# Optimization experiments

Measured on AMD Instinct MI355X. Metric: run time of the kernel, lower is better.

Reference implementation:

```python
import jax, jax.numpy as jnp
import numpy as np
import math

BS, S, D = 2, 2048, 2048
DOWN, UP, H, RD = 512, 1024, 16, 32
HD = D // H            # 128, used only in softmax scale
VD = UP // H           # 64 per-head value dim
CD = UP // H           # 64 per-head content q/k dim
SCALE = math.sqrt(HD) + math.sqrt(RD)


def _rope(x, head_dim):
    # x: [bs, heads, seq, head_dim]; standard rotate-half RoPE
    seq = x.shape[2]
    inv_freq = 1.0 / (10000.0 ** (jnp.arange(0, head_dim, 2, dtype=jnp.float32) / head_dim))
    freqs = jnp.arange(seq, dtype=jnp.float32)[:, None] * inv_freq[None, :]  # [S, hd/2]
    emb = jnp.concatenate([freqs, freqs], axis=-1)                            # [S, hd]
    cos = jnp.cos(emb)[None, None]
    sin = jnp.sin(emb)[None, None]
    x1, x2 = x[..., : head_dim // 2], x[..., head_dim // 2 :]
    rot = jnp.concatenate([-x2, x1], axis=-1)
    return x * cos + rot * sin


def setup_inputs() -> dict:
    key = jax.random.key(0)
    ks = jax.random.split(key, 10)
    sd = 0.02
    inp = {
        'h': jax.random.normal(ks[0], (BS, S, D), jnp.float32),
        'mask': jnp.tril(jnp.ones((1, 1, S, S), jnp.int32)),
        'Wdkv': jax.random.normal(ks[1], (DOWN, D), jnp.float32) * sd,
        'bdkv': jnp.zeros((DOWN,), jnp.float32),
        'Wuk': jax.random.normal(ks[2], (UP, DOWN), jnp.float32) * sd,
        'buk': jnp.zeros((UP,), jnp.float32),
        'Wuv': jax.random.normal(ks[3], (UP, DOWN), jnp.float32) * sd,
        'buv': jnp.zeros((UP,), jnp.float32),
        'Wdq': jax.random.normal(ks[4], (DOWN, D), jnp.float32) * sd,
        'bdq': jnp.zeros((DOWN,), jnp.float32),
        'Wuq': jax.random.normal(ks[5], (UP, DOWN), jnp.float32) * sd,
        'buq': jnp.zeros((UP,), jnp.float32),
        'Wqr': jax.random.normal(ks[6], (RD * H, DOWN), jnp.float32) * sd,
        'bqr': jnp.zeros((RD * H,), jnp.float32),
        'Wkr': jax.random.normal(ks[7], (RD, D), jnp.float32) * sd,
        'bkr': jnp.zeros((RD,), jnp.float32),
        'Wfc': jax.random.normal(ks[8], (D, H * VD), jnp.float32) * sd,
        'bfc': jnp.zeros((D,), jnp.float32),
    }
    return inp


def reference(h, mask, Wdkv, bdkv, Wuk, buk, Wuv, buv, Wdq, bdq, Wuq, buq,
              Wqr, bqr, Wkr, bkr, Wfc, bfc):
    bs, seq, _ = h.shape
    # low-rank KV path
    c_kv = h @ Wdkv.T + bdkv                                   # [bs,S,DOWN]
    k_c = (c_kv @ Wuk.T + buk).reshape(bs, seq, H, CD).transpose(0, 2, 1, 3)
    v_c = (c_kv @ Wuv.T + buv).reshape(bs, seq, H, VD).transpose(0, 2, 1, 3)
    # low-rank Q path
    c_q = h @ Wdq.T + bdq                                      # [bs,S,DOWN]
    q_c = (c_q @ Wuq.T + buq).reshape(bs, seq, H, CD).transpose(0, 2, 1, 3)
    # decoupled RoPE paths
    q_r = _rope((c_q @ Wqr.T + bqr).reshape(bs, seq, H, RD).transpose(0, 2, 1, 3), RD)
    k_r = _rope((h @ Wkr.T + bkr).reshape(bs, seq, 1, RD).transpose(0, 2, 1, 3), RD)
    k_r = jnp.broadcast_to(k_r, (bs, H, seq, RD))              # shared RoPE key across heads
    q = jnp.concatenate([q_c, q_r], axis=-1)                   # [bs,H,S,CD+RD]
    k = jnp.concatenate([k_c, k_r], axis=-1)
    scores = jnp.einsum('bhqd,bhkd->bhqk', q, k)
    # NB: original applies mask BEFORE dividing by scale
    scores = jnp.where(mask == 0, -1e9, scores)
    probs = jax.nn.softmax(scores / SCALE, axis=-1)
    out = jnp.einsum('bhqk,bhkd->bhqd', probs, v_c)            # [bs,H,S,VD]
    out = out.transpose(0, 2, 1, 3).reshape(bs, seq, H * VD)
    return out @ Wfc.T + bfc
```

## Files before the change

### kernel.cpp

```cpp
#include <hip/hip_runtime.h>
#include <hip/hip_bf16.h>
#include <math.h>

typedef unsigned short u16;
typedef __attribute__((ext_vector_type(8))) short bf16x8;
typedef __attribute__((ext_vector_type(4))) float f32x4;
typedef __attribute__((ext_vector_type(16))) float f32x16;

namespace {

constexpr int BS = 2;
constexpr int S = 2048;
constexpr int D = 2048;
constexpr int DOWN = 512;
constexpr int UP = 1024;
constexpr int H = 16;
constexpr int RD = 32;
constexpr int VD = 64;
constexpr int QKD = 96;
constexpr int M = BS * S;
constexpr int N1 = 1152;
constexpr int N2 = 2048;
constexpr int N3 = 1536;

__device__ __forceinline__ float b2f(u16 u) {
  unsigned int x = ((unsigned int)u) << 16;
  return __uint_as_float(x);
}
__device__ __forceinline__ u16 f2b(float f) {
  unsigned int u = __float_as_uint(f);
  u += 0x7fff + ((u >> 16) & 1);
  return (u16)(u >> 16);
}
__device__ __forceinline__ void store_out(float* p, float v) { *p = v; }
__device__ __forceinline__ void store_out(u16* p, float v) { *p = f2b(v); }

__device__ __forceinline__ void async16(const u16* g, u16* lds) {
  __builtin_amdgcn_global_load_lds(
      (const __attribute__((address_space(1))) unsigned int*)g,
      (__attribute__((address_space(3))) unsigned int*)lds, 16, 0, 0);
}

__device__ __forceinline__ float exp2_fast(float x) {
#if __has_builtin(__builtin_amdgcn_exp2f)
  return __builtin_amdgcn_exp2f(x);
#else
  float r;
  asm("v_exp_f32 %0, %1" : "=v"(r) : "v"(x));
  return r;
#endif
}

__device__ __forceinline__ unsigned pkbf(float a, float b) {
  union { __hip_bfloat162 h; unsigned u; } c;
  c.h = __float22bfloat162_rn(make_float2(a, b));
  return c.u;
}
__device__ __forceinline__ void plswap(unsigned& a, unsigned& b) {
  asm("v_permlane32_swap_b32 %0, %1" : "+v"(a), "+v"(b));
}

__device__ __forceinline__ f32x4 mfma32(bf16x8 a, bf16x8 b, f32x4 c) {
  return __builtin_amdgcn_mfma_f32_16x16x32_bf16(a, b, c, 0, 0, 0);
}
__device__ __forceinline__ f32x16 mfma3216(bf16x8 a, bf16x8 b, f32x16 c) {
  return __builtin_amdgcn_mfma_f32_32x32x16_bf16(a, b, c, 0, 0, 0);
}

__global__ __launch_bounds__(256) void prep_kernel(
    const float* __restrict__ h, const float* __restrict__ Wdkv,
    const float* __restrict__ Wdq, const float* __restrict__ Wkr,
    const float* __restrict__ Wuk, const float* __restrict__ Wuv,
    const float* __restrict__ Wuq, const float* __restrict__ Wqr,
    const float* __restrict__ Wfc, const float* __restrict__ bdkv,
    const float* __restrict__ bdq, const float* __restrict__ bkr,
    const float* __restrict__ buk, const float* __restrict__ buv,
    const float* __restrict__ buq, const float* __restrict__ bqr,
    u16* __restrict__ hb, u16* __restrict__ Wcat1, u16* __restrict__ Wcat2,
    u16* __restrict__ Wcat3, u16* __restrict__ Wfcb,
    float* __restrict__ bcat1, float* __restrict__ bcat2,
    float* __restrict__ bcat3, float* __restrict__ ct, float* __restrict__ st) {
  const long i = (long)blockIdx.x * 256 + threadIdx.x;
  if (i >= 3630240) return;
  if (i < 3620864) {
    const float* src; u16* dst; long off;
    if      (i < 2097152) { src = h;    dst = hb;              off = i; }
    else if (i < 2359296) { src = Wdkv; dst = Wcat1;           off = i - 2097152; }
    else if (i < 2621440) { src = Wdq;  dst = Wcat1 + 1048576; off = i - 2359296; }
    else if (i < 2637824) { src = Wkr;  dst = Wcat1 + 2097152; off = i - 2621440; }
    else if (i < 2768896) { src = Wuk;  dst = Wcat2;           off = i - 2637824; }
    else if (i < 2899968) { src = Wuv;  dst = Wcat2 + 524288;  off = i - 2768896; }
    else if (i < 3031040) { src = Wuq;  dst = Wcat3;           off = i - 2899968; }
    else if (i < 3096576) { src = Wqr;  dst = Wcat3 + 524288;  off = i - 3031040; }
    else                  { src = Wfc;  dst = Wfcb;            off = i - 3096576; }
    float4 v = ((const float4*)src)[off];
    ushort4 o;
    o.x = f2b(v.x); o.y = f2b(v.y); o.z = f2b(v.z); o.w = f2b(v.w);
    ((ushort4*)dst)[off] = o;
  } else if (i < 3622048) {
    long j0 = (i - 3620864) * 4;
#pragma unroll
    for (int e = 0; e < 4; ++e) {
      long j = j0 + e;
      if (j < N1) {
        float v = 0.f;
        if (j < 512) v = bdkv[j];
        else if (j < 1024) v = bdq[j - 512];
        else if (j < 1056) v = bkr[j - 1024];
        bcat1[j] = v;
      } else if (j < N1 + N2) {
        long jj = j - N1;
        bcat2[jj] = (jj < 1024) ? buk[jj] : buv[jj - 1024];
      } else {
        long jj = j - N1 - N2;
        bcat3[jj] = (jj < 1024) ? buq[jj] : bqr[jj - 1024];
      }
    }
  } else {
    long k0 = (i - 3622048) * 4;
#pragma unroll
    for (int e = 0; e < 4; ++e) {
      long k = k0 + e;
      int s = (int)(k >> 4), r = (int)(k & 15);
      float f = powf(10000.f, -(float)r / 16.f);
      float th = (float)s * f;
      ct[k] = cosf(th);
      st[k] = sinf(th);
    }
  }
}

template <int BN, typename OutT>
__device__ __forceinline__ void gemm_body(
    const u16* __restrict__ A, int lda, const u16* __restrict__ W, int ldw,
    const float* __restrict__ bias, OutT* __restrict__ C, int ldc, int K,
    int m0, int n0) {
  constexpr int NFR = BN / 32;
  __shared__ u16 As[128 * 32];
  __shared__ u16 Bs[BN * 32];
  const int t = threadIdx.x;
  const int lane = t & 63, wave = t >> 6;
  const int wm = (wave >> 1) * 64, wn = (wave & 1) * (BN / 2);
  const int lrow = lane & 15, lk = (lane >> 4) * 8;
  const int srow = lane >> 2, scol = (lane & 3) * 8;
  f32x4 acc[4][NFR] = {};
  for (int k0 = 0; k0 < K; k0 += 32) {
    __syncthreads();
    {
      int r = wave * 32 + srow;
      async16(A + (size_t)(m0 + r) * lda + k0 + scol, As + (wave * 32) * 32);
      async16(A + (size_t)(m0 + r + 16) * lda + k0 + scol,
              As + (wave * 32 + 16) * 32);
    }
    if (BN == 128) {
      int r = wave * 32 + srow;
      async16(W + (size_t)(n0 + r) * ldw + k0 + scol, Bs + (wave * 32) * 32);
      async16(W + (size_t)(n0 + r + 16) * ldw + k0 + scol,
              Bs + (wave * 32 + 16) * 32);
    } else {
      int r = wave * 16 + srow;
      async16(W + (size_t)(n0 + r) * ldw + k0 + scol, Bs + (wave * 16) * 32);
    }
    __syncthreads();
    bf16x8 af[4], bfr[NFR];
#pragma unroll
    for (int i = 0; i < 4; ++i)
      af[i] = *(const bf16x8*)(As + (wm + i * 16 + lrow) * 32 + lk);
#pragma unroll
    for (int i = 0; i < NFR; ++i)
      bfr[i] = *(const bf16x8*)(Bs + (wn + i * 16 + lrow) * 32 + lk);
#pragma unroll
    for (int mi = 0; mi < 4; ++mi)
#pragma unroll
      for (int ni = 0; ni < NFR; ++ni)
        acc[mi][ni] = mfma32(af[mi], bfr[ni], acc[mi][ni]);
  }
#pragma unroll
  for (int mi = 0; mi < 4; ++mi)
#pragma unroll
    for (int ni = 0; ni < NFR; ++ni)
#pragma unroll
      for (int r = 0; r < 4; ++r) {
        int m = m0 + wm + mi * 16 + (lane >> 4) * 4 + r;
        int n = n0 + wn + ni * 16 + lrow;
        store_out(C + (size_t)m * ldc + n, acc[mi][ni][r] + bias[n]);
      }
}

template <int BN, typename OutT>
__global__ __launch_bounds__(256) void gemm_bt_mfma(
    const u16* __restrict__ A, int lda, const u16* __restrict__ W, int ldw,
    const float* __restrict__ bias, OutT* __restrict__ C, int ldc, int K) {
  gemm_body<BN, OutT>(A, lda, W, ldw, bias, C, ldc, K,
                      blockIdx.x * 128, blockIdx.y * BN);
}

__global__ __launch_bounds__(256) void gemm_up_fused(
    const u16* __restrict__ C1v, const u16* __restrict__ Wcat2,
    const u16* __restrict__ Wcat3, const float* __restrict__ bcat2,
    const float* __restrict__ bcat3, u16* __restrict__ C2,
    u16* __restrict__ C3) {
  const int by = blockIdx.y;
  const u16* A;
  const u16* W;
  const float* bias;
  u16* C;
  int ldc, n0;
  if (by < 16) {
    A = C1v; W = Wcat2; bias = bcat2; C = C2; ldc = N2; n0 = by * 128;
  } else {
    A = C1v + DOWN; W = Wcat3; bias = bcat3; C = C3; ldc = N3;
    n0 = (by - 16) * 128;
  }
  gemm_body<128, u16>(A, N1, W, DOWN, bias, C, ldc, DOWN,
                      blockIdx.x * 128, n0);
}

__global__ __launch_bounds__(256) void transpose_v_kernel(
    const u16* __restrict__ in, int ld_in, u16* __restrict__ VtB) {
  __shared__ u16 tile[64][72];
  const int m0 = blockIdx.x * 64;
  const int h = blockIdx.y;
  const int r = threadIdx.x >> 2, c0 = (threadIdx.x & 3) * 16;
  *(bf16x8*)(&tile[r][c0]) =
      *(const bf16x8*)(in + (size_t)(m0 + r) * ld_in + h * VD + c0);
  *(bf16x8*)(&tile[r][c0 + 8]) =
      *(const bf16x8*)(in + (size_t)(m0 + r) * ld_in + h * VD + c0 + 8);
  __syncthreads();
  bf16x8 o0, o1;
#pragma unroll
  for (int j = 0; j < 8; ++j) {
    o0[j] = (short)tile[c0 + j][r];
    o1[j] = (short)tile[c0 + 8 + j][r];
  }
  const int b = m0 / S, sb = m0 % S;
  size_t dst = ((size_t)(b * H + h) * 64 + ((sb + c0) >> 5)) * 2048 +
               (size_t)r * 32 + ((sb + c0) & 31);
  *(bf16x8*)(VtB + dst) = o0;
  *(bf16x8*)(VtB + dst + 8) = o1;
}

__global__ __launch_bounds__(192) void pack_q_kernel(
    const u16* __restrict__ qc, const u16* __restrict__ qr,
    const float* __restrict__ ct, const float* __restrict__ st,
    u16* __restrict__ Qp) {
  const int t = threadIdx.x;
  const int sub = (t >= 96) ? 1 : 0;
  const int d = t - sub * 96;
  const int s = blockIdx.x * 2 + sub, h = blockIdx.y, b = blockIdx.z;
  const float sc = 1.44269504088896f / (sqrtf(128.f) + sqrtf(32.f));
  float val;
  if (d < 64) {
    val = b2f(qc[(size_t)(b * S + s) * N3 + h * VD + d]);
  } else {
    int r = d - 64;
    const u16* qrow = qr + (size_t)(b * S + s) * N3 + h * RD;
    float x = b2f(qrow[r]), xp = b2f(qrow[r ^ 16]);
    float c = ct[s * 16 + (r & 15)], sn = st[s * 16 + (r & 15)];
    val = (r < 16) ? (x * c - xp * sn) : (x * c + xp * sn);
  }
  Qp[((size_t)(b * H + h) * S + s) * QKD + d] = f2b(val * sc);
}

__global__ __launch_bounds__(192) void pack_k_kernel(
    const u16* __restrict__ kc,
    const u16* __restrict__ kr,
    const float* __restrict__ ct, const float* __restrict__ st,
    u16* __restrict__ Kp) {
  const int t = threadIdx.x;
  const int sub = (t >= 96) ? 1 : 0;
  const int d = t - sub * 96;
  const int s = blockIdx.x * 2 + sub, h = blockIdx.y, b = blockIdx.z;
  float val;
  if (d < 64) {
    val = b2f(kc[(size_t)(b * S + s) * N2 + h * VD + d]);
  } else {
    int r = d - 64;
    const u16* krow = kr + (size_t)(b * S + s) * N1;
    float x = b2f(krow[r]), xp = b2f(krow[r ^ 16]);
    float c = ct[s * 16 + (r & 15)], sn = st[s * 16 + (r & 15)];
    val = (r < 16) ? (x * c - xp * sn) : (x * c + xp * sn);
  }
  Kp[((size_t)(b * H + h) * S + s) * QKD + d] = f2b(val);
}

__global__ __launch_bounds__(256, 3) void attn_mfma(
    const u16* __restrict__ Qp, const u16* __restrict__ Kp,
    const u16* __restrict__ Vt, u16* __restrict__ attnb) {
  const int t = threadIdx.x, wave = t >> 6, lane = t & 63;
  const int l31 = lane & 31, hw = lane >> 5;
  const int xcd = (int)(blockIdx.x & 7), sub = (int)(blockIdx.x >> 3);
  const int bh = xcd * 4 + (sub & 3);
  const int tile = 63 - (sub >> 2);
  const int b = bh >> 4, h = bh & 15;
  const int q0w = tile * 32;
  const size_t hbo = (size_t)bh * S;

  __shared__ float red[3][64][33];

  bf16x8 qf[6];
  {
    const u16* qrow = Qp + (hbo + q0w + l31) * QKD + hw * 8;
#pragma unroll
    for (int c = 0; c < 6; ++c) qf[c] = *(const bf16x8*)(qrow + c * 16);
  }
  f32x16 O0 = {0,0,0,0,0,0,0,0,0,0,0,0,0,0,0,0};
  f32x16 O1 = {0,0,0,0,0,0,0,0,0,0,0,0,0,0,0,0};
  float lsum = 0.f;
  const int q_abs = q0w + l31;
  const u16* vbase = Vt + (size_t)bh * 64 * 2048 + l31 * 32 + 8 * hw;
  const u16* kpb = Kp + hbo * QKD;

  auto qk_part1 = [&](bf16x8* kf, f32x16& sa, f32x16& sb) {
    sa = mfma3216(kf[0], qf[0], sa);
    sb = mfma3216(kf[1], qf[1], sb);
    sa = mfma3216(kf[2], qf[2], sa);
    sb = mfma3216(kf[3], qf[3], sb);
    sa = mfma3216(kf[4], qf[4], sa);
    sb = mfma3216(kf[5], qf[5], sb);
  };
  auto finish = [&](const f32x16& sa, const f32x16& sb, const bf16x8* vf,
                    int m) {
    float e[16];
    if (m == tile) {
      const int k0 = m * 32;
#pragma unroll
      for (int r = 0; r < 16; ++r) {
        int key_abs = k0 + (r & 3) + 8 * (r >> 2) + 4 * hw;
        float v = exp2_fast(sa[r] + sb[r]);
        e[r] = (key_abs <= q_abs) ? v : 0.f;
      }
    } else {
#pragma unroll
      for (int r = 0; r < 16; ++r) e[r] = exp2_fast(sa[r] + sb[r]);
    }
    {
      float p0 = (e[0] + e[1]) + (e[2] + e[3]);
      float p1 = (e[4] + e[5]) + (e[6] + e[7]);
      float p2 = (e[8] + e[9]) + (e[10] + e[11]);
      float p3 = (e[12] + e[13]) + (e[14] + e[15]);
      lsum += (p0 + p1) + (p2 + p3);
    }
    unsigned w0 = pkbf(e[0], e[1]),   w1 = pkbf(e[2], e[3]);
    unsigned w2 = pkbf(e[4], e[5]),   w3 = pkbf(e[6], e[7]);
    unsigned w4 = pkbf(e[8], e[9]),   w5 = pkbf(e[10], e[11]);
    unsigned w6 = pkbf(e[12], e[13]), w7 = pkbf(e[14], e[15]);
    plswap(w0, w2); plswap(w1, w3); plswap(w4, w6); plswap(w5, w7);
    union { unsigned u[4]; bf16x8 v; } ua, ub;
    ua.u[0] = w0; ua.u[1] = w1; ua.u[2] = w2; ua.u[3] = w3;
    ub.u[0] = w4; ub.u[1] = w5; ub.u[2] = w6; ub.u[3] = w7;
    O0 = mfma3216(ua.v, vf[0], O0);
    O1 = mfma3216(ua.v, vf[2], O1);
    O0 = mfma3216(ub.v, vf[1], O0);
    O1 = mfma3216(ub.v, vf[3], O1);
  };
  auto loadK = [&](int m, bf16x8* kf) {
    const u16* kb = kpb + (size_t)(m * 32 + l31) * QKD + hw * 8;
#pragma unroll
    for (int c = 0; c < 6; ++c) kf[c] = *(const bf16x8*)(kb + c * 16);
  };
  auto loadV = [&](int m, bf16x8* vf) {
    const u16* vb = vbase + (size_t)m * 2048;
    vf[0] = *(const bf16x8*)(vb);
    vf[1] = *(const bf16x8*)(vb + 16);
    vf[2] = *(const bf16x8*)(vb + 1024);
    vf[3] = *(const bf16x8*)(vb + 1024 + 16);
  };

  if (tile >= wave) {
    bf16x8 kf[6], vfE[4], vfO[4];
    int m = wave;
    loadK(m, kf);
    loadV(m, vfE);
    while (true) {
      {
        if (m + 4 <= tile) loadV(m + 4, vfO);
        f32x16 sa = {0,0,0,0,0,0,0,0,0,0,0,0,0,0,0,0};
        f32x16 sb = {0,0,0,0,0,0,0,0,0,0,0,0,0,0,0,0};
        qk_part1(kf, sa, sb);
        if (m + 4 <= tile) loadK(m + 4, kf);
        finish(sa, sb, vfE, m);
      }
      m += 4;
      if (m > tile) break;
      {
        if (m + 4 <= tile) loadV(m + 4, vfE);
        f32x16 sa = {0,0,0,0,0,0,0,0,0,0,0,0,0,0,0,0};
        f32x16 sb = {0,0,0,0,0,0,0,0,0,0,0,0,0,0,0,0};
        qk_part1(kf, sa, sb);
        if (m + 4 <= tile) loadK(m + 4, kf);
        finish(sa, sb, vfO, m);
      }
      m += 4;
      if (m > tile) break;
    }
  }

  if (wave > 0) {
#pragma unroll
    for (int r = 0; r < 16; ++r) {
      red[wave - 1][lane][r] = O0[r];
      red[wave - 1][lane][16 + r] = O1[r];
    }
    red[wave - 1][lane][32] = lsum;
  }
  __syncthreads();
  if (wave == 0) {
#pragma unroll
    for (int w = 0; w < 3; ++w) {
#pragma unroll
      for (int r = 0; r < 16; ++r) {
        O0[r] += red[w][lane][r];
        O1[r] += red[w][lane][16 + r];
      }
      lsum += red[w][lane][32];
    }
    float tot = lsum + __shfl_xor(lsum, 32);
    u16* ob = attnb + (size_t)b * S * UP + h * VD;
#pragma unroll
    for (int r = 0; r < 16; ++r) {
      int rowq = (r & 3) + 8 * (r >> 2) + 4 * hw;
      float linv = 1.f / __shfl(tot, rowq);
      size_t rowoff = (size_t)(q0w + rowq) * UP;
      ob[rowoff + l31] = f2b(O0[r] * linv);
      ob[rowoff + 32 + l31] = f2b(O1[r] * linv);
    }
  }
}

}

extern "C" void kernel_launch(void* const* d_in, const int* in_sizes, int n_in,
                              void* d_out, int out_size, void* d_ws, size_t ws_size,
                              hipStream_t stream) {
  const float* h    = (const float*)d_in[0];
  const float* Wdkv = (const float*)d_in[2];
  const float* bdkv = (const float*)d_in[3];
  const float* Wuk  = (const float*)d_in[4];
  const float* buk  = (const float*)d_in[5];
  const float* Wuv  = (const float*)d_in[6];
  const float* buv  = (const float*)d_in[7];
  const float* Wdq  = (const float*)d_in[8];
  const float* bdq  = (const float*)d_in[9];
  const float* Wuq  = (const float*)d_in[10];
  const float* buq  = (const float*)d_in[11];
  const float* Wqr  = (const float*)d_in[12];
  const float* bqr  = (const float*)d_in[13];
  const float* Wkr  = (const float*)d_in[14];
  const float* bkr  = (const float*)d_in[15];
  const float* Wfc  = (const float*)d_in[16];
  const float* bfc  = (const float*)d_in[17];
  float* out = (float*)d_out;

  u16* p = (u16*)d_ws;
  u16* hb    = p; p += (size_t)M * D;
  u16* Wcat1 = p; p += (size_t)N1 * D;
  u16* Wcat2 = p; p += (size_t)N2 * DOWN;
  u16* Wcat3 = p; p += (size_t)N3 * DOWN;
  u16* Wfcb  = p; p += (size_t)D * UP;
  u16* C1    = p; p += (size_t)M * N1;
  u16* C2    = p; p += (size_t)M * N2;
  u16* C3    = p; p += (size_t)M * N3;
  u16* Qp    = p; p += 6291456;
  u16* Kp    = p; p += 6291456;
  u16* Vt    = p; p += (size_t)UP * M;
  float* bcat1 = (float*)p; p += 2 * N1;
  float* bcat2 = (float*)p; p += 2 * N2;
  float* bcat3 = (float*)p; p += 2 * N3;
  float* ct = (float*)p; p += 2 * S * 16;
  float* st = (float*)p; p += 2 * S * 16;
  u16* attnb = C1;

  prep_kernel<<<dim3(14181), 256, 0, stream>>>(
      h, Wdkv, Wdq, Wkr, Wuk, Wuv, Wuq, Wqr, Wfc,
      bdkv, bdq, bkr, buk, buv, buq, bqr,
      hb, Wcat1, Wcat2, Wcat3, Wfcb, bcat1, bcat2, bcat3, ct, st);

  gemm_bt_mfma<128, u16><<<dim3(M / 128, N1 / 128), 256, 0, stream>>>(
      hb, D, Wcat1, D, bcat1, C1, N1, D);
  gemm_up_fused<<<dim3(M / 128, 28), 256, 0, stream>>>(
      C1, Wcat2, Wcat3, bcat2, bcat3, C2, C3);

  pack_q_kernel<<<dim3(S / 2, H, BS), 192, 0, stream>>>(
      C3, C3 + UP, ct, st, Qp);
  pack_k_kernel<<<dim3(S / 2, H, BS), 192, 0, stream>>>(
      C2, C1 + 2 * DOWN, ct, st, Kp);
  transpose_v_kernel<<<dim3(M / 64, UP / 64), 256, 0, stream>>>(
      C2 + UP, N2, Vt);

  attn_mfma<<<dim3(2048), 256, 0, stream>>>(Qp, Kp, Vt, attnb);

  gemm_bt_mfma<128, float><<<dim3(M / 128, D / 128), 256, 0, stream>>>(
      attnb, UP, Wfcb, UP, bfc, out, D, UP);
}
```

Baseline: 318.9 us.

## Merge Q/K pack and V transpose kernels, add setprio around MFMAs, shrink GEMM tile

The Q pack, K pack and V transpose kernels become one flat-indexed launch that uses block ranges to pick the work, which removes two launches and their tail effects. The attention kernel wraps its MFMA groups in s_setprio to raise wave priority during matrix work. The first projection GEMM moves to a 64-wide N tile, doubling its grid for better CU occupancy. The flat indexing adds div/mod by 96 per element, and writes are now contiguous per element while reads become scattered.

```diff
diff --git a/kernel.cpp b/kernel.cpp
--- a/kernel.cpp
+++ b/kernel.cpp
@@ -22,6 +22,7 @@
 constexpr int N1 = 1152;
 constexpr int N2 = 2048;
 constexpr int N3 = 1536;
+constexpr long PACK_ELEMS = (long)BS * H * S * QKD;
 
 __device__ __forceinline__ float b2f(u16 u) {
   unsigned int x = ((unsigned int)u) << 16;
@@ -216,72 +217,72 @@
                       blockIdx.x * 128, n0);
 }
 
-__global__ __launch_bounds__(256) void transpose_v_kernel(
-    const u16* __restrict__ in, int ld_in, u16* __restrict__ VtB) {
-  __shared__ u16 tile[64][72];
-  const int m0 = blockIdx.x * 64;
-  const int h = blockIdx.y;
-  const int r = threadIdx.x >> 2, c0 = (threadIdx.x & 3) * 16;
-  *(bf16x8*)(&tile[r][c0]) =
-      *(const bf16x8*)(in + (size_t)(m0 + r) * ld_in + h * VD + c0);
-  *(bf16x8*)(&tile[r][c0 + 8]) =
-      *(const bf16x8*)(in + (size_t)(m0 + r) * ld_in + h * VD + c0 + 8);
-  __syncthreads();
-  bf16x8 o0, o1;
-#pragma unroll
-  for (int j = 0; j < 8; ++j) {
-    o0[j] = (short)tile[c0 + j][r];
-    o1[j] = (short)tile[c0 + 8 + j][r];
-  }
-  const int b = m0 / S, sb = m0 % S;
-  size_t dst = ((size_t)(b * H + h) * 64 + ((sb + c0) >> 5)) * 2048 +
-               (size_t)r * 32 + ((sb + c0) & 31);
-  *(bf16x8*)(VtB + dst) = o0;
-  *(bf16x8*)(VtB + dst + 8) = o1;
-}
-
-__global__ __launch_bounds__(192) void pack_q_kernel(
+__global__ __launch_bounds__(256) void reshape_kernel(
     const u16* __restrict__ qc, const u16* __restrict__ qr,
-    const float* __restrict__ ct, const float* __restrict__ st,
-    u16* __restrict__ Qp) {
-  const int t = threadIdx.x;
-  const int sub = (t >= 96) ? 1 : 0;
-  const int d = t - sub * 96;
-  const int s = blockIdx.x * 2 + sub, h = blockIdx.y, b = blockIdx.z;
-  const float sc = 1.44269504088896f / (sqrtf(128.f) + sqrtf(32.f));
-  float val;
-  if (d < 64) {
-    val = b2f(qc[(size_t)(b * S + s) * N3 + h * VD + d]);
-  } else {
-    int r = d - 64;
-    const u16* qrow = qr + (size_t)(b * S + s) * N3 + h * RD;
-    float x = b2f(qrow[r]), xp = b2f(qrow[r ^ 16]);
-    float c = ct[s * 16 + (r & 15)], sn = st[s * 16 + (r & 15)];
-    val = (r < 16) ? (x * c - xp * sn) : (x * c + xp * sn);
-  }
-  Qp[((size_t)(b * H + h) * S + s) * QKD + d] = f2b(val * sc);
-}
-
-__global__ __launch_bounds__(192) void pack_k_kernel(
     const u16* __restrict__ kc,
     const u16* __restrict__ kr,
     const float* __restrict__ ct, const float* __restrict__ st,
-    u16* __restrict__ Kp) {
-  const int t = threadIdx.x;
-  const int sub = (t >= 96) ? 1 : 0;
-  const int d = t - sub * 96;
-  const int s = blockIdx.x * 2 + sub, h = blockIdx.y, b = blockIdx.z;
-  float val;
-  if (d < 64) {
-    val = b2f(kc[(size_t)(b * S + s) * N2 + h * VD + d]);
+    const u16* __restrict__ vin,
+    u16* __restrict__ Qp, u16* __restrict__ Kp, u16* __restrict__ VtB) {
+  const int bid = blockIdx.x;
+  if (bid < 49152) {
+    const long i = (long)bid * 256 + threadIdx.x;
+    const int which = (i >= PACK_ELEMS);
+    const long j = which ? i - PACK_ELEMS : i;
+    const int d = (int)(j % 96);
+    const long row = j / 96;
+    const int s = (int)(row & (S - 1));
+    const long hb_ = row >> 11;
+    const int h = (int)(hb_ & 15);
+    const int b = (int)(hb_ >> 4);
+    float val;
+    if (which == 0) {
+      const float sc = 1.44269504088896f / (sqrtf(128.f) + sqrtf(32.f));
+      if (d < 64) {
+        val = b2f(qc[(size_t)(b * S + s) * N3 + h * VD + d]);
+      } else {
+        int r = d - 64;
+        const u16* qrow = qr + (size_t)(b * S + s) * N3 + h * RD;
+        float x = b2f(qrow[r]), xp = b2f(qrow[r ^ 16]);
+        float c = ct[s * 16 + (r & 15)], sn = st[s * 16 + (r & 15)];
+        val = (r < 16) ? (x * c - xp * sn) : (x * c + xp * sn);
+      }
+      Qp[j] = f2b(val * sc);
+    } else {
+      if (d < 64) {
+        val = b2f(kc[(size_t)(b * S + s) * N2 + h * VD + d]);
+      } else {
+        int r = d - 64;
+        const u16* krow = kr + (size_t)(b * S + s) * N1;
+        float x = b2f(krow[r]), xp = b2f(krow[r ^ 16]);
+        float c = ct[s * 16 + (r & 15)], sn = st[s * 16 + (r & 15)];
+        val = (r < 16) ? (x * c - xp * sn) : (x * c + xp * sn);
+      }
+      Kp[j] = f2b(val);
+    }
   } else {
-    int r = d - 64;
-    const u16* krow = kr + (size_t)(b * S + s) * N1;
-    float x = b2f(krow[r]), xp = b2f(krow[r ^ 16]);
-    float c = ct[s * 16 + (r & 15)], sn = st[s * 16 + (r & 15)];
-    val = (r < 16) ? (x * c - xp * sn) : (x * c + xp * sn);
-  }
-  Kp[((size_t)(b * H + h) * S + s) * QKD + d] = f2b(val);
+    __shared__ u16 tile[64][72];
+    const int tb = bid - 49152;
+    const int m0 = (tb & 63) * 64;
+    const int h = tb >> 6;
+    const int r = threadIdx.x >> 2, c0 = (threadIdx.x & 3) * 16;
+    *(bf16x8*)(&tile[r][c0]) =
+        *(const bf16x8*)(vin + (size_t)(m0 + r) * N2 + h * VD + c0);
+    *(bf16x8*)(&tile[r][c0 + 8]) =
+        *(const bf16x8*)(vin + (size_t)(m0 + r) * N2 + h * VD + c0 + 8);
+    __syncthreads();
+    bf16x8 o0, o1;
+#pragma unroll
+    for (int jj = 0; jj < 8; ++jj) {
+      o0[jj] = (short)tile[c0 + jj][r];
+      o1[jj] = (short)tile[c0 + 8 + jj][r];
+    }
+    const int b = m0 / S, sb = m0 % S;
+    size_t dst = ((size_t)(b * H + h) * 64 + ((sb + c0) >> 5)) * 2048 +
+                 (size_t)r * 32 + ((sb + c0) & 31);
+    *(bf16x8*)(VtB + dst) = o0;
+    *(bf16x8*)(VtB + dst + 8) = o1;
+  }
 }
 
 __global__ __launch_bounds__(256, 3) void attn_mfma(
@@ -312,12 +313,14 @@
   const u16* kpb = Kp + hbo * QKD;
 
   auto qk_part1 = [&](bf16x8* kf, f32x16& sa, f32x16& sb) {
+    __builtin_amdgcn_s_setprio(1);
     sa = mfma3216(kf[0], qf[0], sa);
     sb = mfma3216(kf[1], qf[1], sb);
     sa = mfma3216(kf[2], qf[2], sa);
     sb = mfma3216(kf[3], qf[3], sb);
     sa = mfma3216(kf[4], qf[4], sa);
     sb = mfma3216(kf[5], qf[5], sb);
+    __builtin_amdgcn_s_setprio(0);
   };
   auto finish = [&](const f32x16& sa, const f32x16& sb, const bf16x8* vf,
                     int m) {
@@ -349,10 +352,12 @@
     union { unsigned u[4]; bf16x8 v; } ua, ub;
     ua.u[0] = w0; ua.u[1] = w1; ua.u[2] = w2; ua.u[3] = w3;
     ub.u[0] = w4; ub.u[1] = w5; ub.u[2] = w6; ub.u[3] = w7;
+    __builtin_amdgcn_s_setprio(1);
     O0 = mfma3216(ua.v, vf[0], O0);
     O1 = mfma3216(ua.v, vf[2], O1);
     O0 = mfma3216(ub.v, vf[1], O0);
     O1 = mfma3216(ub.v, vf[3], O1);
+    __builtin_amdgcn_s_setprio(0);
   };
   auto loadK = [&](int m, bf16x8* kf) {
     const u16* kb = kpb + (size_t)(m * 32 + l31) * QKD + hw * 8;
@@ -476,17 +481,13 @@
       bdkv, bdq, bkr, buk, buv, buq, bqr,
       hb, Wcat1, Wcat2, Wcat3, Wfcb, bcat1, bcat2, bcat3, ct, st);
 
-  gemm_bt_mfma<128, u16><<<dim3(M / 128, N1 / 128), 256, 0, stream>>>(
+  gemm_bt_mfma<64, u16><<<dim3(M / 128, N1 / 64), 256, 0, stream>>>(
       hb, D, Wcat1, D, bcat1, C1, N1, D);
   gemm_up_fused<<<dim3(M / 128, 28), 256, 0, stream>>>(
       C1, Wcat2, Wcat3, bcat2, bcat3, C2, C3);
 
-  pack_q_kernel<<<dim3(S / 2, H, BS), 192, 0, stream>>>(
-      C3, C3 + UP, ct, st, Qp);
-  pack_k_kernel<<<dim3(S / 2, H, BS), 192, 0, stream>>>(
-      C2, C1 + 2 * DOWN, ct, st, Kp);
-  transpose_v_kernel<<<dim3(M / 64, UP / 64), 256, 0, stream>>>(
-      C2 + UP, N2, Vt);
+  reshape_kernel<<<dim3(50176), 256, 0, stream>>>(
+      C3, C3 + UP, C2, C1 + 2 * DOWN, ct, st, C2 + UP, Qp, Kp, Vt);
 
   attn_mfma<<<dim3(2048), 256, 0, stream>>>(Qp, Kp, Vt, attnb);
 
```

Result: no change. 315.9 us (-1.0%).
